# Optimization experiments

Measured on AMD Instinct MI355X. Metric: run time of the kernel, lower is better.

## Reference

```python
import jax, jax.numpy as jnp
import numpy as np

N, T, n, C, C2 = 4, 8, 16384, 64, 64

def setup_inputs() -> dict:
    key = jax.random.key(0)
    k1, k2, k3, k4, k5 = jax.random.split(key, 5)
    return {
        "key_mem": jax.random.normal(k1, (N, T, n, C), dtype=jnp.float32),
        "val_mem": jax.random.normal(k2, (N, T, n, C2), dtype=jnp.float32),
        "key_cur": jax.random.normal(k3, (N, n, C), dtype=jnp.float32),
        "val_cur": jax.random.normal(k4, (N, n, C2), dtype=jnp.float32),
        "alpha": jax.random.normal(k5, (1,), dtype=jnp.float32),
    }

def reference(key_mem, val_mem, key_cur, val_cur, alpha):
    # kv_mul: contract memory tokens (T*n) -> (N, C, C2), tiny matrix
    kv_mul = jnp.einsum('btnc,btnd->bcd', key_mem, val_mem)
    # softmax over the C axis (dim=1 in torch layout (N, C, C2))
    kv_mul = jax.nn.softmax(kv_mul, axis=1)
    # out: (N, n, C) @ (N, C, C2) -> (N, n, C2)
    out = jnp.einsum('bnc,bcd->bnd', key_cur, kv_mul)
    return alpha * out + val_cur
```

## Files before the change

kernel.cpp:

```cpp
#include <hip/hip_runtime.h>
#include <math.h>

#define N_TOK   16384
#define K_TOT   (8 * N_TOK)
#define N_BATCH 4
#define BPB     128
#define RPB     (K_TOT / BPB)
#define CHUNK   64
#define NCH     (RPB / CHUNK)
#define PITCH_U 36
#define PART_U  (64 * PITCH_U)

typedef short short8 __attribute__((ext_vector_type(8)));
typedef float f32x4  __attribute__((ext_vector_type(4)));

union FragU { uint4 u; short8 s; };

__device__ __forceinline__ uint bf16_rne(float f, float* rounded) {
  uint u = __float_as_uint(f);
  uint r = u + 0x7FFFu + ((u >> 16) & 1u);
  *rounded = __uint_as_float(r & 0xFFFF0000u);
  return r >> 16;
}

__global__ __launch_bounds__(512, 2) void k1_mfma(
    const float* __restrict__ key, const float* __restrict__ val,
    float* __restrict__ part) {
  __shared__ uint lds[4 * PART_U];

  int blk  = blockIdx.x;
  int b    = blk / BPB;
  int p    = blk % BPB;
  int t    = threadIdx.x;
  int wave = t >> 6;
  int lane = t & 63;

  int arr = t >> 8;
  int tt  = t & 255;
  int c0  = (tt & 15) * 4;
  int r0  = (tt >> 4) * 4;
  const float* src = arr ? val : key;
  size_t rowbase = (size_t)b * K_TOT + (size_t)p * RPB;
  uint sbase = arr * 2 * PART_U;

  int mt  = wave >> 1;
  int ntb = (wave & 1) * 2;
  int m16 = lane & 15;
  int ko  = lane >> 4;

  f32x4 acc[2] = {{0.f, 0.f, 0.f, 0.f}, {0.f, 0.f, 0.f, 0.f}};
  float4 ld[4];

  auto load_chunk = [&](int ch) {
#pragma unroll
    for (int q = 0; q < 4; q++)
      ld[q] = *(const float4*)&src[(rowbase + (size_t)ch * CHUNK + r0 + q) * 64 + c0];
  };

  auto write_chunk = [&]() {
#pragma unroll
    for (int cc = 0; cc < 4; cc++) {
      uint h[4], l[4];
#pragma unroll
      for (int q = 0; q < 4; q++) {
        float f = (&ld[q].x)[cc];
        float hf;
        h[q] = bf16_rne(f, &hf);
        float dummy;
        l[q] = bf16_rne(f - hf, &dummy);
      }
      uint2 hp = make_uint2(h[0] | (h[1] << 16), h[2] | (h[3] << 16));
      uint2 lp = make_uint2(l[0] | (l[1] << 16), l[2] | (l[3] << 16));
      uint base = sbase + (uint)(c0 + cc) * PITCH_U + (uint)(r0 >> 1);
      *(uint2*)&lds[base]          = hp;
      *(uint2*)&lds[base + PART_U] = lp;
    }
  };

  load_chunk(0);
  write_chunk();
  __syncthreads();

  for (int ch = 0; ch < NCH; ch++) {
    if (ch + 1 < NCH) load_chunk(ch + 1);

#pragma unroll
    for (int ks = 0; ks < 2; ks++) {
      uint ao = (uint)(mt * 16 + m16) * PITCH_U + ks * 16 + ko * 4;
      FragU Ah, Al;
      Ah.u = *(const uint4*)&lds[ao];
      Al.u = *(const uint4*)&lds[ao + PART_U];
#pragma unroll
      for (int nn = 0; nn < 2; nn++) {
        uint bo = 2 * PART_U + (uint)((ntb + nn) * 16 + m16) * PITCH_U + ks * 16 + ko * 4;
        FragU Bh, Bl;
        Bh.u = *(const uint4*)&lds[bo];
        Bl.u = *(const uint4*)&lds[bo + PART_U];
        acc[nn] = __builtin_amdgcn_mfma_f32_16x16x32_bf16(Ah.s, Bh.s, acc[nn], 0, 0, 0);
        acc[nn] = __builtin_amdgcn_mfma_f32_16x16x32_bf16(Ah.s, Bl.s, acc[nn], 0, 0, 0);
        acc[nn] = __builtin_amdgcn_mfma_f32_16x16x32_bf16(Al.s, Bh.s, acc[nn], 0, 0, 0);
      }
    }
    __syncthreads();
    if (ch + 1 < NCH) write_chunk();
    __syncthreads();
  }

  float* dst = part + (size_t)blk * 4096;
#pragma unroll
  for (int nn = 0; nn < 2; nn++) {
    int d = (ntb + nn) * 16 + m16;
#pragma unroll
    for (int r = 0; r < 4; r++) {
      int c = mt * 16 + ko * 4 + r;
      dst[c * 64 + d] = acc[nn][r];
    }
  }
}

__global__ __launch_bounds__(256, 4) void k2_reduce(
    const float* __restrict__ part, float* __restrict__ kv, int bpb) {
  int b  = blockIdx.x >> 6;
  int c  = blockIdx.x & 63;
  int p4 = threadIdx.x >> 6;
  int d  = threadIdx.x & 63;

  float s = 0.f;
  int iters = bpb >> 2;
  const float* src = part + (size_t)(b * bpb) * 4096 + c * 64 + d;
#pragma unroll 4
  for (int x = 0; x < iters; x++) s += src[(size_t)(p4 + 4 * x) * 4096];

  __shared__ float l[256];
  l[threadIdx.x] = s;
  __syncthreads();
  if (p4 == 0)
    kv[((size_t)b * 64 + c) * 64 + d] = l[d] + l[64 + d] + l[128 + d] + l[192 + d];
}

__global__ __launch_bounds__(64, 4) void k2b_softmax(
    const float* __restrict__ kv, float* __restrict__ P) {
  int b = blockIdx.x >> 6;
  int d = blockIdx.x & 63;
  int c = threadIdx.x;
  float v = kv[(size_t)b * 4096 + c * 64 + d];
  float mx = v;
#pragma unroll
  for (int o = 32; o; o >>= 1) mx = fmaxf(mx, __shfl_xor(mx, o, 64));
  float e = __expf(v - mx);
  float s = e;
#pragma unroll
  for (int o = 32; o; o >>= 1) s += __shfl_xor(s, o, 64);
  P[(size_t)b * 4096 + c * 64 + d] = e / s;
}

__global__ __launch_bounds__(256, 4) void k3_out(
    const float* __restrict__ P, const float* __restrict__ keyc,
    const float* __restrict__ valc, const float* __restrict__ alphap,
    float* __restrict__ out) {
  __shared__ float Ps[4096];
  __shared__ float kT[64 * 68];

  int bb = blockIdx.x >> 8;
  int mb = blockIdx.x & 255;
  int m0 = mb * 64;
  int t = threadIdx.x;

  const float4* p4 = (const float4*)(P + (size_t)bb * 4096);
  float4* ps4 = (float4*)Ps;
#pragma unroll
  for (int u = 0; u < 4; u++) ps4[t + 256 * u] = p4[t + 256 * u];

  int r  = t >> 2;
  int cb = (t & 3) * 16;
  const float* krow = keyc + ((size_t)bb * N_TOK + m0 + r) * 64;
#pragma unroll
  for (int u = 0; u < 4; u++) {
    float4 kk = *(const float4*)&krow[cb + 4 * u];
    int c = cb + 4 * u;
    kT[(c + 0) * 68 + r] = kk.x;
    kT[(c + 1) * 68 + r] = kk.y;
    kT[(c + 2) * 68 + r] = kk.z;
    kT[(c + 3) * 68 + r] = kk.w;
  }
  __syncthreads();

  int wave = t >> 6, lane = t & 63;
  int mi = lane >> 3, j = lane & 7;
  int m = wave * 16 + mi * 2;

  float acc[2][8];
#pragma unroll
  for (int a = 0; a < 2; a++)
#pragma unroll
    for (int d = 0; d < 8; d++) acc[a][d] = 0.f;

#pragma unroll 4
  for (int c = 0; c < 64; c++) {
    float2 kk = *(const float2*)&kT[c * 68 + m];
    float4 p0 = *(const float4*)&Ps[c * 64 + 8 * j];
    float4 p1 = *(const float4*)&Ps[c * 64 + 8 * j + 4];
    float pr[8] = {p0.x, p0.y, p0.z, p0.w, p1.x, p1.y, p1.z, p1.w};
#pragma unroll
    for (int d = 0; d < 8; d++) {
      acc[0][d] = fmaf(kk.x, pr[d], acc[0][d]);
      acc[1][d] = fmaf(kk.y, pr[d], acc[1][d]);
    }
  }

  float alpha = alphap[0];
#pragma unroll
  for (int a = 0; a < 2; a++) {
    size_t off = ((size_t)bb * N_TOK + m0 + m + a) * 64 + 8 * j;
    float4 v0 = *(const float4*)&valc[off];
    float4 v1 = *(const float4*)&valc[off + 4];
    float4 o0 = make_float4(fmaf(alpha, acc[a][0], v0.x),
                            fmaf(alpha, acc[a][1], v0.y),
                            fmaf(alpha, acc[a][2], v0.z),
                            fmaf(alpha, acc[a][3], v0.w));
    float4 o1 = make_float4(fmaf(alpha, acc[a][4], v1.x),
                            fmaf(alpha, acc[a][5], v1.y),
                            fmaf(alpha, acc[a][6], v1.z),
                            fmaf(alpha, acc[a][7], v1.w));
    *(float4*)&out[off] = o0;
    *(float4*)&out[off + 4] = o1;
  }
}

extern "C" void kernel_launch(void* const* d_in, const int* in_sizes, int n_in,
                              void* d_out, int out_size, void* d_ws,
                              size_t ws_size, hipStream_t stream) {
  const float* key_mem = (const float*)d_in[0];
  const float* val_mem = (const float*)d_in[1];
  const float* key_cur = (const float*)d_in[2];
  const float* val_cur = (const float*)d_in[3];
  const float* alpha   = (const float*)d_in[4];
  float* out = (float*)d_out;
  float* ws  = (float*)d_ws;

  float* part = ws;
  float* kv   = ws + (size_t)(N_BATCH * BPB) * 4096;
  float* P    = ws;

  k1_mfma<<<N_BATCH * BPB, 512, 0, stream>>>(key_mem, val_mem, part);
  k2_reduce<<<256, 256, 0, stream>>>(part, kv, BPB);
  k2b_softmax<<<N_BATCH * 64, 64, 0, stream>>>(kv, P);
  k3_out<<<N_BATCH * (N_TOK / 64), 256, 0, stream>>>(P, key_cur, val_cur,
                                                     alpha, out);
}
```

Measured before the change: 322.3 us.

## Double-buffer LDS and registers in k1 with a non-draining barrier

Splits the k1 LDS staging area into two buffers and keeps two register sets of prefetched chunks, so global loads run two chunks ahead. Each iteration now needs one barrier instead of two. A custom barrier waits only on LDS counters, not outstanding global loads, so those loads can stay in flight across it. In exchange, LDS use per block doubles (about 73KB), which may limit occupancy, register pressure rises, and the loop is fully unrolled.

After: 319.6 us. About the same (-0.8%).

```diff
diff --git a/kernel.cpp b/kernel.cpp
--- a/kernel.cpp
+++ b/kernel.cpp
@@ -23,10 +23,17 @@
   return r >> 16;
 }
 
+__device__ __forceinline__ void barrier_nodrain() {
+  asm volatile("" ::: "memory");
+  __builtin_amdgcn_s_waitcnt(0xC07F);
+  __builtin_amdgcn_s_barrier();
+  asm volatile("" ::: "memory");
+}
+
 __global__ __launch_bounds__(512, 2) void k1_mfma(
     const float* __restrict__ key, const float* __restrict__ val,
     float* __restrict__ part) {
-  __shared__ uint lds[4 * PART_U];
+  __shared__ uint lds[2][4 * PART_U];
 
   int blk  = blockIdx.x;
   int b    = blk / BPB;
@@ -49,21 +56,22 @@
   int ko  = lane >> 4;
 
   f32x4 acc[2] = {{0.f, 0.f, 0.f, 0.f}, {0.f, 0.f, 0.f, 0.f}};
-  float4 ld[4];
-
-  auto load_chunk = [&](int ch) {
+  float4 ld[2][4];
+
+  auto load_chunk = [&](int ch, int par) {
 #pragma unroll
     for (int q = 0; q < 4; q++)
-      ld[q] = *(const float4*)&src[(rowbase + (size_t)ch * CHUNK + r0 + q) * 64 + c0];
+      ld[par][q] =
+          *(const float4*)&src[(rowbase + (size_t)ch * CHUNK + r0 + q) * 64 + c0];
   };
 
-  auto write_chunk = [&]() {
+  auto write_chunk = [&](int par) {
 #pragma unroll
     for (int cc = 0; cc < 4; cc++) {
       uint h[4], l[4];
 #pragma unroll
       for (int q = 0; q < 4; q++) {
-        float f = (&ld[q].x)[cc];
+        float f = (&ld[par][q].x)[cc];
         float hf;
         h[q] = bf16_rne(f, &hf);
         float dummy;
@@ -72,38 +80,43 @@
       uint2 hp = make_uint2(h[0] | (h[1] << 16), h[2] | (h[3] << 16));
       uint2 lp = make_uint2(l[0] | (l[1] << 16), l[2] | (l[3] << 16));
       uint base = sbase + (uint)(c0 + cc) * PITCH_U + (uint)(r0 >> 1);
-      *(uint2*)&lds[base]          = hp;
-      *(uint2*)&lds[base + PART_U] = lp;
+      *(uint2*)&lds[par][base]          = hp;
+      *(uint2*)&lds[par][base + PART_U] = lp;
     }
   };
 
-  load_chunk(0);
-  write_chunk();
-  __syncthreads();
-
-  for (int ch = 0; ch < NCH; ch++) {
-    if (ch + 1 < NCH) load_chunk(ch + 1);
-
+  auto compute = [&](int par) {
 #pragma unroll
     for (int ks = 0; ks < 2; ks++) {
       uint ao = (uint)(mt * 16 + m16) * PITCH_U + ks * 16 + ko * 4;
       FragU Ah, Al;
-      Ah.u = *(const uint4*)&lds[ao];
-      Al.u = *(const uint4*)&lds[ao + PART_U];
+      Ah.u = *(const uint4*)&lds[par][ao];
+      Al.u = *(const uint4*)&lds[par][ao + PART_U];
 #pragma unroll
       for (int nn = 0; nn < 2; nn++) {
-        uint bo = 2 * PART_U + (uint)((ntb + nn) * 16 + m16) * PITCH_U + ks * 16 + ko * 4;
+        uint bo = 2 * PART_U + (uint)((ntb + nn) * 16 + m16) * PITCH_U +
+                  ks * 16 + ko * 4;
         FragU Bh, Bl;
-        Bh.u = *(const uint4*)&lds[bo];
-        Bl.u = *(const uint4*)&lds[bo + PART_U];
+        Bh.u = *(const uint4*)&lds[par][bo];
+        Bl.u = *(const uint4*)&lds[par][bo + PART_U];
         acc[nn] = __builtin_amdgcn_mfma_f32_16x16x32_bf16(Ah.s, Bh.s, acc[nn], 0, 0, 0);
         acc[nn] = __builtin_amdgcn_mfma_f32_16x16x32_bf16(Ah.s, Bl.s, acc[nn], 0, 0, 0);
         acc[nn] = __builtin_amdgcn_mfma_f32_16x16x32_bf16(Al.s, Bh.s, acc[nn], 0, 0, 0);
       }
     }
-    __syncthreads();
-    if (ch + 1 < NCH) write_chunk();
-    __syncthreads();
+  };
+
+  load_chunk(0, 0);
+  load_chunk(1, 1);
+  write_chunk(0);
+  barrier_nodrain();
+
+#pragma unroll
+  for (int ch = 0; ch < NCH; ch++) {
+    if (ch + 2 < NCH) load_chunk(ch + 2, ch & 1);
+    compute(ch & 1);
+    if (ch + 1 < NCH) write_chunk((ch + 1) & 1);
+    barrier_nodrain();
   }
 
   float* dst = part + (size_t)blk * 4096;
```
